# Optimization experiments

Measured on AMD Instinct MI355X. Metric: run time of the kernel, lower is better.

## Reference

```python
import jax, jax.numpy as jnp
import numpy as np

D_MODEL = 1024
NHEAD = 16
D_K = D_MODEL // NHEAD


def setup_inputs() -> dict:
    key = jax.random.key(0)
    ks = jax.random.split(key, 11)
    B, S = 2, 2048
    scale = 1.0 / np.sqrt(D_MODEL)
    inp = {
        "q": jax.random.normal(ks[0], (B, S, D_MODEL), jnp.float32),
        "k": jax.random.normal(ks[1], (B, S, D_MODEL), jnp.float32),
        "v": jax.random.normal(ks[2], (B, S, D_MODEL), jnp.float32),
        "Wq": jax.random.normal(ks[3], (D_MODEL, D_MODEL), jnp.float32) * scale,
        "bq": jnp.zeros((D_MODEL,), jnp.float32),
        "Wk": jax.random.normal(ks[4], (D_MODEL, D_MODEL), jnp.float32) * scale,
        "bk": jnp.zeros((D_MODEL,), jnp.float32),
        "Wv": jax.random.normal(ks[5], (D_MODEL, D_MODEL), jnp.float32) * scale,
        "bv": jnp.zeros((D_MODEL,), jnp.float32),
        "Wo": jax.random.normal(ks[6], (D_MODEL, D_MODEL), jnp.float32) * scale,
        "bo": jnp.zeros((D_MODEL,), jnp.float32),
    }
    return inp


def reference(q, k, v, Wq, bq, Wk, bk, Wv, bv, Wo, bo):
    B, S, _ = q.shape
    # Linear projections (torch Linear: x @ W.T + b), split into heads
    def proj(x, W, b):
        y = jnp.einsum('bsd,ed->bse', x, W) + b
        return y.reshape(B, -1, NHEAD, D_K).transpose(0, 2, 1, 3)  # [B,H,S,Dk]

    qh = proj(q, Wq, bq)
    kh = proj(k, Wk, bk)
    vh = proj(v, Wv, bv)

    scores = jnp.einsum('bhqd,bhkd->bhqk', qh, kh) / jnp.sqrt(
        jnp.asarray(D_K, qh.dtype))
    attn = jax.nn.softmax(scores, axis=-1)  # dropout is identity in eval
    out = jnp.einsum('bhqk,bhkd->bhqd', attn, vh)
    out = out.transpose(0, 2, 1, 3).reshape(B, S, D_MODEL)
    return jnp.einsum('bsd,ed->bse', out, Wo) + bo
```

## Files before the change

kernel.cpp:

```cpp
#include <hip/hip_runtime.h>
#include <stdint.h>
#include <stddef.h>

#define D_MODEL 1024
#define NHEAD   16
#define DK      64
#define BB      2
#define SS      2048
#define NTOK    (BB*SS)

#define SCALE_Q 0.18033688011f

typedef short  short8 __attribute__((ext_vector_type(8)));
typedef __bf16 bf16x8 __attribute__((ext_vector_type(8)));
typedef float  f32x4  __attribute__((ext_vector_type(4)));

__device__ __forceinline__ unsigned short f2bf(float x){
  unsigned int u = __builtin_bit_cast(unsigned int, x);
  u += 0x7fffu + ((u >> 16) & 1u);
  return (unsigned short)(u >> 16);
}

__device__ __forceinline__ unsigned int pack_bf2(float x, float y){
  unsigned int a = __builtin_bit_cast(unsigned int, x) + 0x8000u;
  unsigned int b = __builtin_bit_cast(unsigned int, y) + 0x8000u;
  return __builtin_amdgcn_perm(b, a, 0x07060302u);
}

__device__ __forceinline__ float fast_exp2(float x){
#if __has_builtin(__builtin_amdgcn_exp2f)
  return __builtin_amdgcn_exp2f(x);
#else
  return exp2f(x);
#endif
}

__device__ __forceinline__ f32x4 mfma16(bf16x8 a, bf16x8 b, f32x4 c){
  return __builtin_amdgcn_mfma_f32_16x16x32_bf16(a, b, c, 0, 0, 0);
}

__device__ __forceinline__ void async16(const void* g, void* lds){
  __builtin_amdgcn_global_load_lds(
      (const __attribute__((address_space(1))) unsigned int*)g,
      (__attribute__((address_space(3))) unsigned int*)lds,
      16, 0, 0);
}

__global__ __launch_bounds__(256) void cast_bf16_all(
    const float* __restrict__ q,  const float* __restrict__ k,  const float* __restrict__ v,
    const float* __restrict__ wq, const float* __restrict__ wk, const float* __restrict__ wv,
    const float* __restrict__ wo,
    unsigned short* __restrict__ qb,  unsigned short* __restrict__ kb,  unsigned short* __restrict__ vb,
    unsigned short* __restrict__ wqb, unsigned short* __restrict__ wkb, unsigned short* __restrict__ wvb,
    unsigned short* __restrict__ wob)
{
  const float* src; unsigned short* dst; int n;
  switch (blockIdx.y){
    case 0: src = q;  dst = qb;  n = NTOK*D_MODEL;    break;
    case 1: src = k;  dst = kb;  n = NTOK*D_MODEL;    break;
    case 2: src = v;  dst = vb;  n = NTOK*D_MODEL;    break;
    case 3: src = wq; dst = wqb; n = D_MODEL*D_MODEL; break;
    case 4: src = wk; dst = wkb; n = D_MODEL*D_MODEL; break;
    case 5: src = wv; dst = wvb; n = D_MODEL*D_MODEL; break;
    default: src = wo; dst = wob; n = D_MODEL*D_MODEL; break;
  }
  int i = (blockIdx.x * 256 + threadIdx.x) * 8;
  if (i >= n) return;
  float4 a = *(const float4*)(src + i);
  float4 b = *(const float4*)(src + i + 4);
  short8 o;
  o[0] = (short)f2bf(a.x); o[1] = (short)f2bf(a.y);
  o[2] = (short)f2bf(a.z); o[3] = (short)f2bf(a.w);
  o[4] = (short)f2bf(b.x); o[5] = (short)f2bf(b.y);
  o[6] = (short)f2bf(b.z); o[7] = (short)f2bf(b.w);
  *(short8*)(dst + i) = o;
}

__global__ __launch_bounds__(256) void qkv_gemm(
    const unsigned short* __restrict__ qb, const unsigned short* __restrict__ kb,
    const unsigned short* __restrict__ vb,
    const unsigned short* __restrict__ wqb, const unsigned short* __restrict__ wkb,
    const unsigned short* __restrict__ wvb,
    const float* __restrict__ bq, const float* __restrict__ bk, const float* __restrict__ bv,
    unsigned short* __restrict__ Qh, unsigned short* __restrict__ Kh, unsigned short* __restrict__ Vt)
{
  __shared__ __align__(16) unsigned short As[128*64];
  __shared__ __align__(16) unsigned short Bs[128*64];
  const int id = blockIdx.x, z = id >> 8, r = id & 255;
  const unsigned short *A, *Bt; const float* bias; unsigned short* C;
  int bm, bn, N, brow; float scale;
  if (z == 0){ A = qb;  Bt = wqb; bias = bq; C = Qh; bm = (r>>3)*128; bn = (r&7)*128; N = 1024; brow = 0; scale = SCALE_Q; }
  else if (z == 1){ A = kb;  Bt = wkb; bias = bk; C = Kh; bm = (r>>3)*128; bn = (r&7)*128; N = 1024; brow = 0; scale = 1.0f; }
  else            { A = wvb; Bt = vb;  bias = bv; C = Vt; bm = (r&7)*128; bn = (r>>3)*128; N = 4096; brow = 1; scale = 1.0f; }
  const int K = 1024;
  const int tid  = threadIdx.x, lane = tid & 63, w = tid >> 6;
  const int quad = lane >> 4,   l16  = lane & 15;
  const int wm = w >> 1, wn = w & 1;
  const int sw = l16 & 7;
  f32x4 acc[4][4] = {};
  for (int kb_ = 0; kb_ < 16; ++kb_){
    const int k0 = kb_ << 6;
    __syncthreads();
    #pragma unroll
    for (int c = 0; c < 4; ++c){
      int chunk = (w*4 + c)*64 + lane;
      int row = chunk >> 3, c8 = chunk & 7;
      int cs = (c8 ^ (row & 7)) << 3;
      async16(A  + (size_t)(bm + row)*K + k0 + cs, (char*)As + (w*4 + c)*1024);
      async16(Bt + (size_t)(bn + row)*K + k0 + cs, (char*)Bs + (w*4 + c)*1024);
    }
    __syncthreads();
    bf16x8 af[4][2], bf[4][2];
    #pragma unroll
    for (int mt = 0; mt < 4; ++mt)
      #pragma unroll
      for (int ks = 0; ks < 2; ++ks){
        int off = (((ks*4 + quad) ^ sw) << 3);
        af[mt][ks] = *(const bf16x8*)&As[(wm*64 + mt*16 + l16)*64 + off];
        bf[mt][ks] = *(const bf16x8*)&Bs[(wn*64 + mt*16 + l16)*64 + off];
      }
    #pragma unroll
    for (int ks = 0; ks < 2; ++ks)
      #pragma unroll
      for (int mt = 0; mt < 4; ++mt)
        #pragma unroll
        for (int nt = 0; nt < 4; ++nt)
          acc[mt][nt] = mfma16(af[mt][ks], bf[nt][ks], acc[mt][nt]);
  }
  const int m0 = bm + wm*64, n0 = bn + wn*64;
  #pragma unroll
  for (int mt = 0; mt < 4; ++mt){
    #pragma unroll
    for (int nt = 0; nt < 4; ++nt){
      int col = n0 + nt*16 + l16;
      float bc = brow ? 0.0f : bias[col];
      #pragma unroll
      for (int rr = 0; rr < 4; ++rr){
        int row = m0 + mt*16 + quad*4 + rr;
        float val = (acc[mt][nt][rr] + (brow ? bias[row] : bc)) * scale;
        C[(size_t)row*N + col] = f2bf(val);
      }
    }
  }
}

__global__ __launch_bounds__(256) void gemm_out(
    const unsigned short* __restrict__ A, const unsigned short* __restrict__ Bt,
    const float* __restrict__ bias, float* __restrict__ C)
{
  __shared__ __align__(16) unsigned short As[64*64];
  __shared__ __align__(16) unsigned short Bs[128*64];
  const int K = 1024, N = 1024;
  const int tid  = threadIdx.x, lane = tid & 63, w = tid >> 6;
  const int quad = lane >> 4,   l16  = lane & 15;
  const int bm = blockIdx.y * 64, bn = blockIdx.x * 128;
  const int sw = l16 & 7;
  f32x4 acc[4][2] = {};
  for (int kb_ = 0; kb_ < 16; ++kb_){
    const int k0 = kb_ << 6;
    __syncthreads();
    #pragma unroll
    for (int c = 0; c < 2; ++c){
      int chunk = (w*2 + c)*64 + lane;
      int row = chunk >> 3, c8 = chunk & 7;
      async16(A + (size_t)(bm + row)*K + k0 + ((c8 ^ (row & 7)) << 3),
              (char*)As + (w*2 + c)*1024);
    }
    #pragma unroll
    for (int c = 0; c < 4; ++c){
      int chunk = (w*4 + c)*64 + lane;
      int row = chunk >> 3, c8 = chunk & 7;
      async16(Bt + (size_t)(bn + row)*K + k0 + ((c8 ^ (row & 7)) << 3),
              (char*)Bs + (w*4 + c)*1024);
    }
    __syncthreads();
    bf16x8 af[4][2], bf[2][2];
    #pragma unroll
    for (int mt = 0; mt < 4; ++mt)
      #pragma unroll
      for (int ks = 0; ks < 2; ++ks)
        af[mt][ks] = *(const bf16x8*)&As[(mt*16 + l16)*64 + (((ks*4 + quad) ^ sw) << 3)];
    #pragma unroll
    for (int nt = 0; nt < 2; ++nt)
      #pragma unroll
      for (int ks = 0; ks < 2; ++ks)
        bf[nt][ks] = *(const bf16x8*)&Bs[(w*32 + nt*16 + l16)*64 + (((ks*4 + quad) ^ sw) << 3)];
    #pragma unroll
    for (int ks = 0; ks < 2; ++ks)
      #pragma unroll
      for (int mt = 0; mt < 4; ++mt)
        #pragma unroll
        for (int nt = 0; nt < 2; ++nt)
          acc[mt][nt] = mfma16(af[mt][ks], bf[nt][ks], acc[mt][nt]);
  }
  #pragma unroll
  for (int mt = 0; mt < 4; ++mt){
    #pragma unroll
    for (int nt = 0; nt < 2; ++nt){
      int col = bn + w*32 + nt*16 + l16;
      float bc = bias[col];
      #pragma unroll
      for (int rr = 0; rr < 4; ++rr){
        int row = bm + mt*16 + quad*4 + rr;
        C[(size_t)row*N + col] = acc[mt][nt][rr] + bc;
      }
    }
  }
}

__global__ __launch_bounds__(256) void attn(
    const unsigned short* __restrict__ Qh, const unsigned short* __restrict__ Kh,
    const unsigned short* __restrict__ Vt,
    float* __restrict__ Op, float* __restrict__ lp)
{
  __shared__ __align__(16) char smem[32768];
  unsigned short* Kbuf = (unsigned short*)smem;
  unsigned short* Vbuf = (unsigned short*)(smem + 8192);
  unsigned short* QP   = (unsigned short*)(smem + 16384);

  const int tid  = threadIdx.x, lane = tid & 63, w = tid >> 6;
  const int quad = lane >> 4,   l16  = lane & 15;
  const int bh = blockIdx.y, b = bh >> 4, h = bh & 15;
  const int q0 = blockIdx.x * 128;
  const int part = blockIdx.z;
  const int sw = l16 & 7;

  #pragma unroll
  for (int c = 0; c < 4; ++c){
    int s = (w*4 + c)*64 + lane;
    int row = s >> 3, c8 = s & 7;
    async16(Qh + (size_t)(b*SS + q0 + row)*D_MODEL + h*DK + ((c8 ^ (row & 7)) << 3),
            (char*)QP + (w*4 + c)*1024);
  }
  __syncthreads();
  bf16x8 bq[2][2];
  #pragma unroll
  for (int qg = 0; qg < 2; ++qg)
    #pragma unroll
    for (int ks = 0; ks < 2; ++ks)
      bq[qg][ks] = *(const bf16x8*)&QP[(w*32 + qg*16 + l16)*64 + (((ks*4 + quad) ^ sw) << 3)];

  const unsigned short* Kp = Kh + (size_t)(b*SS)*D_MODEL + h*DK;
  const unsigned short* Vp = Vt + (size_t)(h*DK)*NTOK + b*SS;
  const unsigned short* ksrc[2];
  const unsigned short* vsrc[2];
  #pragma unroll
  for (int c = 0; c < 2; ++c){
    int s = (w*2 + c)*64 + lane;
    int row = s >> 3, c8 = s & 7;
    int cs = (c8 ^ (row & 7)) << 3;
    ksrc[c] = Kp + (size_t)(part*1024 + row)*D_MODEL + cs;
    vsrc[c] = Vp + (size_t)row*NTOK + part*1024 + cs;
  }

  f32x4 acc[2][4] = {};
  float l_i[2] = {0.0f, 0.0f};

  for (int it = 0; it < 16; ++it){
    __syncthreads();
    #pragma unroll
    for (int c = 0; c < 2; ++c){
      async16(ksrc[c], (char*)Kbuf + (w*2 + c)*1024);
      async16(vsrc[c], (char*)Vbuf + (w*2 + c)*1024);
      ksrc[c] += 64*D_MODEL;
      vsrc[c] += 64;
    }
    __syncthreads();

    bf16x8 kf[4][2];
    #pragma unroll
    for (int mt = 0; mt < 4; ++mt)
      #pragma unroll
      for (int ks = 0; ks < 2; ++ks)
        kf[mt][ks] = *(const bf16x8*)&Kbuf[(mt*16 + l16)*64 + (((ks*4 + quad) ^ sw) << 3)];
    f32x4 s0[4] = {}, s1[4] = {};
    #pragma unroll
    for (int mt = 0; mt < 4; ++mt)
      #pragma unroll
      for (int ks = 0; ks < 2; ++ks){
        s0[mt] = mfma16(kf[mt][ks], bq[0][ks], s0[mt]);
        s1[mt] = mfma16(kf[mt][ks], bq[1][ks], s1[mt]);
      }

    float ls0 = 0.0f, ls1 = 0.0f;
    #pragma unroll
    for (int mt = 0; mt < 4; ++mt)
      #pragma unroll
      for (int rr = 0; rr < 4; ++rr){
        float p0 = fast_exp2(s0[mt][rr]); s0[mt][rr] = p0; ls0 += p0;
        float p1 = fast_exp2(s1[mt][rr]); s1[mt][rr] = p1; ls1 += p1;
      }
    l_i[0] += ls0; l_i[1] += ls1;
    const int pr0 = (w*32 +      l16)*64;
    const int pr1 = (w*32 + 16 + l16)*64;
    #pragma unroll
    for (int mt = 0; mt < 4; ++mt){
      int c8  = mt*2 + (quad >> 1);
      int off = ((c8 ^ sw) << 3) + (quad & 1)*4;
      uint2 p;
      p.x = pack_bf2(s0[mt][0], s0[mt][1]);
      p.y = pack_bf2(s0[mt][2], s0[mt][3]);
      *(uint2*)&QP[pr0 + off] = p;
      p.x = pack_bf2(s1[mt][0], s1[mt][1]);
      p.y = pack_bf2(s1[mt][2], s1[mt][3]);
      *(uint2*)&QP[pr1 + off] = p;
    }
    asm volatile("s_waitcnt lgkmcnt(0)" ::: "memory");

    bf16x8 bp[2][2];
    #pragma unroll
    for (int qg = 0; qg < 2; ++qg)
      #pragma unroll
      for (int ks = 0; ks < 2; ++ks)
        bp[qg][ks] = *(const bf16x8*)&QP[(w*32 + qg*16 + l16)*64 + (((ks*4 + quad) ^ sw) << 3)];
    bf16x8 vf[4][2];
    #pragma unroll
    for (int nt = 0; nt < 4; ++nt)
      #pragma unroll
      for (int ks = 0; ks < 2; ++ks)
        vf[nt][ks] = *(const bf16x8*)&Vbuf[(nt*16 + l16)*64 + (((ks*4 + quad) ^ sw) << 3)];
    #pragma unroll
    for (int nt = 0; nt < 4; ++nt)
      #pragma unroll
      for (int ks = 0; ks < 2; ++ks){
        acc[0][nt] = mfma16(vf[nt][ks], bp[0][ks], acc[0][nt]);
        acc[1][nt] = mfma16(vf[nt][ks], bp[1][ks], acc[1][nt]);
      }
  }

  float lred[2];
  #pragma unroll
  for (int qg = 0; qg < 2; ++qg){
    float t = l_i[qg];
    t += __shfl_xor(t, 16);
    t += __shfl_xor(t, 32);
    lred[qg] = t;
  }
  if (quad == 0){
    #pragma unroll
    for (int qg = 0; qg < 2; ++qg)
      lp[(size_t)part*(32*SS) + (size_t)bh*SS + q0 + w*32 + qg*16 + l16] = lred[qg];
  }

  float* F = (float*)smem;
  float* myOp = Op + (size_t)part*((size_t)32*SS*DK) + ((size_t)bh*SS + q0)*DK;
  #pragma unroll
  for (int ph = 0; ph < 2; ++ph){
    __syncthreads();
    if ((w >> 1) == ph){
      #pragma unroll
      for (int qg = 0; qg < 2; ++qg){
        int fr = (w & 1)*32 + qg*16 + l16;
        #pragma unroll
        for (int nt = 0; nt < 4; ++nt)
          *(f32x4*)&F[fr*68 + nt*16 + quad*4] = acc[qg][nt];
      }
    }
    __syncthreads();
    int row = tid >> 2, cb = (tid & 3)*16;
    float* dst = myOp + (size_t)(ph*64 + row)*DK;
    #pragma unroll
    for (int i = 0; i < 4; ++i)
      *(f32x4*)(dst + cb + i*4) = *(const f32x4*)&F[row*68 + cb + i*4];
  }
}

__global__ __launch_bounds__(256) void combine(
    const float* __restrict__ Op, const float* __restrict__ lp,
    unsigned short* __restrict__ ctx)
{
  const size_t OPS = (size_t)32*SS*DK;
  int t = blockIdx.x;
  int b = t >> 11, s = t & (SS-1);
  int f = threadIdx.x * 4;
  int h = f >> 6, dk = f & 63;
  size_t o = ((size_t)(b*16 + h)*SS + s)*DK + dk;
  f32x4 o0 = *(const f32x4*)&Op[o];
  f32x4 o1 = *(const f32x4*)&Op[OPS + o];
  size_t li = (size_t)(b*16 + h)*SS + s;
  float inv = 1.0f / (lp[li] + lp[(size_t)32*SS + li]);
  uint2 r;
  r.x = pack_bf2((o0[0]+o1[0])*inv, (o0[1]+o1[1])*inv);
  r.y = pack_bf2((o0[2]+o1[2])*inv, (o0[3]+o1[3])*inv);
  *(uint2*)&ctx[(size_t)t*D_MODEL + f] = r;
}

extern "C" void kernel_launch(void* const* d_in, const int* in_sizes, int n_in,
                              void* d_out, int out_size, void* d_ws, size_t ws_size,
                              hipStream_t stream) {
  const float* q  = (const float*)d_in[0];
  const float* k  = (const float*)d_in[1];
  const float* v  = (const float*)d_in[2];
  const float* Wq = (const float*)d_in[3];
  const float* bq = (const float*)d_in[4];
  const float* Wk = (const float*)d_in[5];
  const float* bk = (const float*)d_in[6];
  const float* Wv = (const float*)d_in[7];
  const float* bv = (const float*)d_in[8];
  const float* Wo = (const float*)d_in[9];
  const float* bo = (const float*)d_in[10];

  const size_t MB = 1024*1024;
  char* ws = (char*)d_ws;
  unsigned short* wob = (unsigned short*)(ws);
  unsigned short* Qh  = (unsigned short*)(ws + 2*MB);
  unsigned short* Kh  = (unsigned short*)(ws + 10*MB);
  unsigned short* Vt  = (unsigned short*)(ws + 18*MB);
  unsigned short* ctx = (unsigned short*)(ws + 26*MB);
  float*          lp  = (float*)(ws + 34*MB);
  char* S = ws + 35*MB;
  unsigned short* qb  = (unsigned short*)(S);
  unsigned short* kb  = (unsigned short*)(S + 8*MB);
  unsigned short* vb  = (unsigned short*)(S + 16*MB);
  unsigned short* wqb = (unsigned short*)(S + 24*MB);
  unsigned short* wkb = (unsigned short*)(S + 26*MB);
  unsigned short* wvb = (unsigned short*)(S + 28*MB);
  float*          Op  = (float*)(S);

  cast_bf16_all<<<dim3(2048, 7), 256, 0, stream>>>(q, k, v, Wq, Wk, Wv, Wo,
                                                   qb, kb, vb, wqb, wkb, wvb, wob);
  qkv_gemm<<<dim3(768), 256, 0, stream>>>(qb, kb, vb, wqb, wkb, wvb,
                                          bq, bk, bv, Qh, Kh, Vt);
  attn<<<dim3(SS/128, BB*NHEAD, 2), 256, 0, stream>>>(Qh, Kh, Vt, Op, lp);
  combine<<<dim3(NTOK), 256, 0, stream>>>(Op, lp, ctx);
  gemm_out<<<dim3(8, 64), 256, 0, stream>>>(ctx, wob, bo, (float*)d_out);
}
```

Baseline: 243.4 us.

## Double attention query tile per block to 256 rows for K/V reuse

Each attention block now handles 256 query rows instead of 128: each wave owns 64 queries, processed as four 16-row groups per K/V tile. This halves the number of blocks and the global/LDS traffic for loading K and V per query, and enlarges shared memory to 48KB for the bigger Q/P buffer. In exchange, register pressure rises (acc doubles), the grid shrinks to 512 blocks, which may underfill the GPU, and the epilogue needs more serialized phases.

```diff
diff --git a/kernel.cpp b/kernel.cpp
--- a/kernel.cpp
+++ b/kernel.cpp
@@ -208,12 +208,12 @@
   }
 }
 
-__global__ __launch_bounds__(256) void attn(
+__global__ __launch_bounds__(256, 2) void attn(
     const unsigned short* __restrict__ Qh, const unsigned short* __restrict__ Kh,
     const unsigned short* __restrict__ Vt,
     float* __restrict__ Op, float* __restrict__ lp)
 {
-  __shared__ __align__(16) char smem[32768];
+  __shared__ __align__(16) char smem[49152];
   unsigned short* Kbuf = (unsigned short*)smem;
   unsigned short* Vbuf = (unsigned short*)(smem + 8192);
   unsigned short* QP   = (unsigned short*)(smem + 16384);
@@ -221,24 +221,24 @@
   const int tid  = threadIdx.x, lane = tid & 63, w = tid >> 6;
   const int quad = lane >> 4,   l16  = lane & 15;
   const int bh = blockIdx.y, b = bh >> 4, h = bh & 15;
-  const int q0 = blockIdx.x * 128;
+  const int q0 = blockIdx.x * 256;
   const int part = blockIdx.z;
   const int sw = l16 & 7;
 
   #pragma unroll
-  for (int c = 0; c < 4; ++c){
-    int s = (w*4 + c)*64 + lane;
+  for (int c = 0; c < 8; ++c){
+    int s = (w*8 + c)*64 + lane;
     int row = s >> 3, c8 = s & 7;
     async16(Qh + (size_t)(b*SS + q0 + row)*D_MODEL + h*DK + ((c8 ^ (row & 7)) << 3),
-            (char*)QP + (w*4 + c)*1024);
+            (char*)QP + (w*8 + c)*1024);
   }
   __syncthreads();
-  bf16x8 bq[2][2];
-  #pragma unroll
-  for (int qg = 0; qg < 2; ++qg)
+  bf16x8 bq[4][2];
+  #pragma unroll
+  for (int qg = 0; qg < 4; ++qg)
     #pragma unroll
     for (int ks = 0; ks < 2; ++ks)
-      bq[qg][ks] = *(const bf16x8*)&QP[(w*32 + qg*16 + l16)*64 + (((ks*4 + quad) ^ sw) << 3)];
+      bq[qg][ks] = *(const bf16x8*)&QP[(w*64 + qg*16 + l16)*64 + (((ks*4 + quad) ^ sw) << 3)];
 
   const unsigned short* Kp = Kh + (size_t)(b*SS)*D_MODEL + h*DK;
   const unsigned short* Vp = Vt + (size_t)(h*DK)*NTOK + b*SS;
@@ -253,8 +253,8 @@
     vsrc[c] = Vp + (size_t)row*NTOK + part*1024 + cs;
   }
 
-  f32x4 acc[2][4] = {};
-  float l_i[2] = {0.0f, 0.0f};
+  f32x4 acc[4][4] = {};
+  float l_i[4] = {0.0f, 0.0f, 0.0f, 0.0f};
 
   for (int it = 0; it < 16; ++it){
     __syncthreads();
@@ -273,46 +273,36 @@
       #pragma unroll
       for (int ks = 0; ks < 2; ++ks)
         kf[mt][ks] = *(const bf16x8*)&Kbuf[(mt*16 + l16)*64 + (((ks*4 + quad) ^ sw) << 3)];
-    f32x4 s0[4] = {}, s1[4] = {};
-    #pragma unroll
-    for (int mt = 0; mt < 4; ++mt)
-      #pragma unroll
-      for (int ks = 0; ks < 2; ++ks){
-        s0[mt] = mfma16(kf[mt][ks], bq[0][ks], s0[mt]);
-        s1[mt] = mfma16(kf[mt][ks], bq[1][ks], s1[mt]);
+
+    #pragma unroll
+    for (int qg = 0; qg < 4; ++qg){
+      f32x4 s[4] = {};
+      #pragma unroll
+      for (int mt = 0; mt < 4; ++mt)
+        #pragma unroll
+        for (int ks = 0; ks < 2; ++ks)
+          s[mt] = mfma16(kf[mt][ks], bq[qg][ks], s[mt]);
+      float ls = 0.0f;
+      #pragma unroll
+      for (int mt = 0; mt < 4; ++mt)
+        #pragma unroll
+        for (int rr = 0; rr < 4; ++rr){
+          float p = fast_exp2(s[mt][rr]); s[mt][rr] = p; ls += p;
+        }
+      l_i[qg] += ls;
+      const int pr = (w*64 + qg*16 + l16)*64;
+      #pragma unroll
+      for (int mt = 0; mt < 4; ++mt){
+        int c8  = mt*2 + (quad >> 1);
+        int off = ((c8 ^ sw) << 3) + (quad & 1)*4;
+        uint2 p;
+        p.x = pack_bf2(s[mt][0], s[mt][1]);
+        p.y = pack_bf2(s[mt][2], s[mt][3]);
+        *(uint2*)&QP[pr + off] = p;
       }
-
-    float ls0 = 0.0f, ls1 = 0.0f;
-    #pragma unroll
-    for (int mt = 0; mt < 4; ++mt)
-      #pragma unroll
-      for (int rr = 0; rr < 4; ++rr){
-        float p0 = fast_exp2(s0[mt][rr]); s0[mt][rr] = p0; ls0 += p0;
-        float p1 = fast_exp2(s1[mt][rr]); s1[mt][rr] = p1; ls1 += p1;
-      }
-    l_i[0] += ls0; l_i[1] += ls1;
-    const int pr0 = (w*32 +      l16)*64;
-    const int pr1 = (w*32 + 16 + l16)*64;
-    #pragma unroll
-    for (int mt = 0; mt < 4; ++mt){
-      int c8  = mt*2 + (quad >> 1);
-      int off = ((c8 ^ sw) << 3) + (quad & 1)*4;
-      uint2 p;
-      p.x = pack_bf2(s0[mt][0], s0[mt][1]);
-      p.y = pack_bf2(s0[mt][2], s0[mt][3]);
-      *(uint2*)&QP[pr0 + off] = p;
-      p.x = pack_bf2(s1[mt][0], s1[mt][1]);
-      p.y = pack_bf2(s1[mt][2], s1[mt][3]);
-      *(uint2*)&QP[pr1 + off] = p;
     }
     asm volatile("s_waitcnt lgkmcnt(0)" ::: "memory");
 
-    bf16x8 bp[2][2];
-    #pragma unroll
-    for (int qg = 0; qg < 2; ++qg)
-      #pragma unroll
-      for (int ks = 0; ks < 2; ++ks)
-        bp[qg][ks] = *(const bf16x8*)&QP[(w*32 + qg*16 + l16)*64 + (((ks*4 + quad) ^ sw) << 3)];
     bf16x8 vf[4][2];
     #pragma unroll
     for (int nt = 0; nt < 4; ++nt)
@@ -320,45 +310,47 @@
       for (int ks = 0; ks < 2; ++ks)
         vf[nt][ks] = *(const bf16x8*)&Vbuf[(nt*16 + l16)*64 + (((ks*4 + quad) ^ sw) << 3)];
     #pragma unroll
-    for (int nt = 0; nt < 4; ++nt)
-      #pragma unroll
-      for (int ks = 0; ks < 2; ++ks){
-        acc[0][nt] = mfma16(vf[nt][ks], bp[0][ks], acc[0][nt]);
-        acc[1][nt] = mfma16(vf[nt][ks], bp[1][ks], acc[1][nt]);
-      }
-  }
-
-  float lred[2];
-  #pragma unroll
-  for (int qg = 0; qg < 2; ++qg){
+    for (int qg = 0; qg < 4; ++qg){
+      bf16x8 bp[2];
+      #pragma unroll
+      for (int ks = 0; ks < 2; ++ks)
+        bp[ks] = *(const bf16x8*)&QP[(w*64 + qg*16 + l16)*64 + (((ks*4 + quad) ^ sw) << 3)];
+      #pragma unroll
+      for (int nt = 0; nt < 4; ++nt)
+        #pragma unroll
+        for (int ks = 0; ks < 2; ++ks)
+          acc[qg][nt] = mfma16(vf[nt][ks], bp[ks], acc[qg][nt]);
+    }
+  }
+
+  #pragma unroll
+  for (int qg = 0; qg < 4; ++qg){
     float t = l_i[qg];
     t += __shfl_xor(t, 16);
     t += __shfl_xor(t, 32);
-    lred[qg] = t;
+    l_i[qg] = t;
   }
   if (quad == 0){
     #pragma unroll
-    for (int qg = 0; qg < 2; ++qg)
-      lp[(size_t)part*(32*SS) + (size_t)bh*SS + q0 + w*32 + qg*16 + l16] = lred[qg];
+    for (int qg = 0; qg < 4; ++qg)
+      lp[(size_t)part*(32*SS) + (size_t)bh*SS + q0 + w*64 + qg*16 + l16] = l_i[qg];
   }
 
   float* F = (float*)smem;
   float* myOp = Op + (size_t)part*((size_t)32*SS*DK) + ((size_t)bh*SS + q0)*DK;
   #pragma unroll
-  for (int ph = 0; ph < 2; ++ph){
-    __syncthreads();
-    if ((w >> 1) == ph){
-      #pragma unroll
-      for (int qg = 0; qg < 2; ++qg){
-        int fr = (w & 1)*32 + qg*16 + l16;
+  for (int p = 0; p < 4; ++p){
+    __syncthreads();
+    if (w == p){
+      #pragma unroll
+      for (int qg = 0; qg < 4; ++qg)
         #pragma unroll
         for (int nt = 0; nt < 4; ++nt)
-          *(f32x4*)&F[fr*68 + nt*16 + quad*4] = acc[qg][nt];
-      }
+          *(f32x4*)&F[(qg*16 + l16)*68 + nt*16 + quad*4] = acc[qg][nt];
     }
     __syncthreads();
     int row = tid >> 2, cb = (tid & 3)*16;
-    float* dst = myOp + (size_t)(ph*64 + row)*DK;
+    float* dst = myOp + (size_t)(p*64 + row)*DK;
     #pragma unroll
     for (int i = 0; i < 4; ++i)
       *(f32x4*)(dst + cb + i*4) = *(const f32x4*)&F[row*68 + cb + i*4];
@@ -421,7 +413,7 @@
                                                    qb, kb, vb, wqb, wkb, wvb, wob);
   qkv_gemm<<<dim3(768), 256, 0, stream>>>(qb, kb, vb, wqb, wkb, wvb,
                                           bq, bk, bv, Qh, Kh, Vt);
-  attn<<<dim3(SS/128, BB*NHEAD, 2), 256, 0, stream>>>(Qh, Kh, Vt, Op, lp);
+  attn<<<dim3(SS/256, BB*NHEAD, 2), 256, 0, stream>>>(Qh, Kh, Vt, Op, lp);
   combine<<<dim3(NTOK), 256, 0, stream>>>(Op, lp, ctx);
   gemm_out<<<dim3(8, 64), 256, 0, stream>>>(ctx, wob, bo, (float*)d_out);
 }
```

After: 243.7 us. No clear change (+0.1%).
